# Kernel optimization log

Hardware: AMD Instinct MI355X
Metric: run time of the kernel (lower is better)

The kernel has to match this reference:

```python
import jax, jax.numpy as jnp
import numpy as np

MUL = 32          # multiplicity of 0e and 1o channels
NRAD = 8          # radial basis size
NPATH = 7         # TP instructions

# Orthonormal symmetric-traceless basis for the real l=2 irrep -> Cartesian map
_B = np.zeros((5, 3, 3))
_s2 = 1.0 / np.sqrt(2.0)
_B[0, 0, 1] = _B[0, 1, 0] = _s2                      # xy
_B[1, 1, 2] = _B[1, 2, 1] = _s2                      # yz
_B[2] = np.diag([-1.0, -1.0, 2.0]) / np.sqrt(6.0)    # 2z^2-x^2-y^2
_B[3, 0, 2] = _B[3, 2, 0] = _s2                      # xz
_B[4] = np.diag([1.0, -1.0, 0.0]) / np.sqrt(2.0)     # x^2-y^2
# w3j(1,2,1)[i,M,k], Frobenius-normalized to 1 (e3nn convention)
C121 = jnp.asarray(np.transpose(_B, (1, 0, 2)) / np.sqrt(5.0), jnp.float32)
INV_SQRT3 = float(1.0 / np.sqrt(3.0))   # w3j(1,1,0) / w3j(0,1,1) / w3j(1,0,1)
A0 = float(1.0 / np.sqrt(64.0))         # path weight, l=0 outs: sqrt(1/fan_in), fan_in=2*32
A1 = float(np.sqrt(3.0 / 96.0))         # path weight, l=1 out: sqrt((2l+1)/fan_in), fan_in=3*32


def setup_inputs() -> dict:
    key = jax.random.key(0)
    ks = jax.random.split(key, 9)
    N, E = 4096, 32768
    x = jax.random.normal(ks[0], (N, 4 * MUL), jnp.float32)
    edge_attr = jax.random.normal(ks[1], (E, 9), jnp.float32)
    edge_length = jax.random.uniform(ks[2], (E,), jnp.float32) * 5.0
    edge_src = jax.random.randint(ks[3], (E,), 0, N)
    edge_dst = jax.random.randint(ks[4], (E,), 0, N)
    W_fc1 = jax.random.normal(ks[5], (NRAD, 64), jnp.float32)
    W_fc2 = jax.random.normal(ks[6], (64, NPATH * MUL * MUL), jnp.float32)
    W_sc_s = jax.random.normal(ks[7], (MUL, MUL), jnp.float32)
    W_sc_v = jax.random.normal(ks[8], (MUL, MUL), jnp.float32)
    return dict(x=x, edge_attr=edge_attr, edge_length=edge_length,
                edge_src=edge_src, edge_dst=edge_dst,
                W_fc1=W_fc1, W_fc2=W_fc2, W_sc_s=W_sc_s, W_sc_v=W_sc_v)


def reference(x, edge_attr, edge_length, edge_src, edge_dst, W_fc1, W_fc2, W_sc_s, W_sc_v):
    N = x.shape[0]
    # radial Gaussian basis: centers linspace(0,5,8), sigma = spacing
    centers = jnp.linspace(0.0, 5.0, NRAD)
    sigma = 5.0 / (NRAD - 1)
    d = edge_length[:, None] - centers[None, :]
    radial = jnp.exp(-d * d / (2.0 * sigma * sigma))
    # radial MLP -> per-edge TP weights (e3nn FullyConnectedNet: W/sqrt(fan_in), silu)
    h = jax.nn.silu(radial @ (W_fc1 / jnp.sqrt(jnp.float32(NRAD))))
    w = h @ (W_fc2 / jnp.sqrt(jnp.float32(64)))          # [E, 7168]
    W = w.reshape(-1, NPATH, MUL, MUL)                    # [E,7,u,w]
    # split node features: 32x0e scalars + 32x1o vectors
    s = x[:, :MUL]
    v = x[:, MUL:].reshape(N, MUL, 3)
    sj = s[edge_src]                                      # [E,u]
    vj = v[edge_src]                                      # [E,u,3]
    y0 = edge_attr[:, 0]
    y1 = edge_attr[:, 1:4]
    y2 = edge_attr[:, 4:9]
    # tensor-product paths
    t00 = sj * y0[:, None]                                            # 0e x 0e
    t11 = jnp.einsum('eui,ei->eu', vj, y1) * INV_SQRT3                # 1o x 1o -> 0e
    out_s = (jnp.einsum('eu,euw->ew', t00, W[:, 0]) +
             jnp.einsum('eu,euw->ew', t11, W[:, 1])) * A0             # scalars
    out_g = (jnp.einsum('eu,euw->ew', t00, W[:, 2]) +
             jnp.einsum('eu,euw->ew', t11, W[:, 3])) * A0             # gates
    t01 = sj[:, :, None] * y1[:, None, :] * INV_SQRT3                 # 0e x 1o -> 1o
    t10 = vj * (y0[:, None, None] * INV_SQRT3)                        # 1o x 0e -> 1o
    t12 = jnp.einsum('eui,imk,em->euk', vj, C121, y2)                 # 1o x 2e -> 1o
    out_v = (jnp.einsum('euk,euw->ewk', t01, W[:, 4]) +
             jnp.einsum('euk,euw->ewk', t10, W[:, 5]) +
             jnp.einsum('euk,euw->ewk', t12, W[:, 6])) * A1           # [E,w,3]
    m_ij = jnp.concatenate([out_s, out_g, out_v.reshape(-1, 3 * MUL)], axis=1)  # [E,160]
    # scatter-mean over destination nodes
    sums = jax.ops.segment_sum(m_ij, edge_dst, num_segments=N)
    cnt = jax.ops.segment_sum(jnp.ones((m_ij.shape[0],), m_ij.dtype), edge_dst, num_segments=N)
    m_i = sums / jnp.clip(cnt, 1.0)[:, None]
    # gate: silu on scalars, sigmoid gates multiply the 1o block per-channel
    gs = jax.nn.silu(m_i[:, :MUL])
    gate = jax.nn.sigmoid(m_i[:, MUL:2 * MUL])
    gv = m_i[:, 2 * MUL:].reshape(N, MUL, 3) * gate[:, :, None]
    # residual self-connection (e3nn o3.Linear: per-irrep, / sqrt(mul_in))
    inv_sqrt_mul = 1.0 / jnp.sqrt(jnp.float32(MUL))
    h_s = gs + (s @ W_sc_s) * inv_sqrt_mul
    h_v = gv + jnp.einsum('nui,uw->nwi', v, W_sc_v) * inv_sqrt_mul
    # o3.Norm: per-irrep L2 norm over the (2l+1) components
    norm_s = jnp.sqrt(h_s * h_s + 1e-12)
    norm_v = jnp.sqrt(jnp.sum(h_v * h_v, axis=-1) + 1e-12)
    return jnp.concatenate([norm_s, norm_v], axis=1)       # [N, 64]
```

## Files before the change

kernel.cpp:

```cpp
#include <hip/hip_runtime.h>

#define NIVL  256
#define KINV  51.2f
#define KSTEP 0.01953125f
#define TPW   7168
#define BCAP  256
#define DCAP  64
#define NROW  11
#define TSTR  40
#define TPACK 448

typedef __attribute__((ext_vector_type(8))) __bf16 bf16x8;
typedef __attribute__((ext_vector_type(4))) float f32x4;
union FragU { uint4 u; bf16x8 v; };

__device__ __forceinline__ float sigmoidf_(float v) { return 1.f / (1.f + expf(-v)); }
__device__ __forceinline__ unsigned bf16r_(float x) { return (__float_as_uint(x) + 0x8000u) >> 16; }
__device__ __forceinline__ unsigned pk_(float lo, float hi) { return (bf16r_(hi) << 16) | bf16r_(lo); }

__device__ __forceinline__ f32x4 mfma_(bf16x8 a, bf16x8 b, f32x4 c) {
    return __builtin_amdgcn_mfma_f32_16x16x32_bf16(a, b, c, 0, 0, 0);
}

__global__ __launch_bounds__(256)
void prep_kernel(const float* __restrict__ W1, const float* __restrict__ W2,
                 const float* __restrict__ elen, const int* __restrict__ esrc,
                 const int* __restrict__ edst, const float* __restrict__ ea,
                 uint4* __restrict__ Bpk, int* __restrict__ cntL, int* __restrict__ cntD,
                 float* __restrict__ erec, int* __restrict__ sortedD, int E)
{
    __shared__ float hk_s[5][64];
    __shared__ float Tsl[5][1024];
    const int tid = threadIdx.x;
    const int vb = blockIdx.x;
    if (vb < TPACK) {
        const int bx = vb % 7;
        const int k0 = (vb / 7) * 4;
        for (int idx = tid; idx < 320; idx += 256) {
            int kk = idx >> 6, c = idx & 63;
            float L = (float)(k0 + kk) * KSTEP;
            float d = 0.f;
#pragma unroll
            for (int r = 0; r < 8; ++r) {
                float dd = L - (float)r * (5.f / 7.f);
                d += expf(-dd * dd * 0.98f) * W1[r * 64 + c];
            }
            d *= 0.3535533906f;
            hk_s[kk][c] = d * sigmoidf_(d) * 0.125f;
        }
        __syncthreads();
        float4 acc[5];
#pragma unroll
        for (int q = 0; q < 5; ++q) acc[q] = make_float4(0.f, 0.f, 0.f, 0.f);
        const int pw = bx * 1024 + tid * 4;
#pragma unroll 4
        for (int c = 0; c < 64; ++c) {
            float4 w4 = *(const float4*)(W2 + (size_t)c * TPW + pw);
#pragma unroll
            for (int q = 0; q < 5; ++q) {
                float hv = hk_s[q][c];
                acc[q].x = fmaf(hv, w4.x, acc[q].x);
                acc[q].y = fmaf(hv, w4.y, acc[q].y);
                acc[q].z = fmaf(hv, w4.z, acc[q].z);
                acc[q].w = fmaf(hv, w4.w, acc[q].w);
            }
        }
        __syncthreads();
#pragma unroll
        for (int q = 0; q < 5; ++q)
            *(float4*)&Tsl[q][tid * 4] = acc[q];
        __syncthreads();
        const int lane_s = tid & 63, whs = (tid >> 6) & 1, ih = tid >> 7;
        const int u0p = (lane_s >> 4) * 8, wp = whs * 16 + (lane_s & 15);
#pragma unroll
        for (int t2 = 0; t2 < 2; ++t2) {
            const int jj = k0 + ih + t2 * 2;
            const int kk = jj - k0;
            unsigned ta[4], dd[4];
#pragma unroll
            for (int q = 0; q < 4; ++q) {
                float a0 = Tsl[kk][(u0p + 2 * q) * 32 + wp];
                float a1 = Tsl[kk][(u0p + 2 * q + 1) * 32 + wp];
                float b0 = Tsl[kk + 1][(u0p + 2 * q) * 32 + wp];
                float b1 = Tsl[kk + 1][(u0p + 2 * q + 1) * 32 + wp];
                ta[q] = pk_(a0, a1);
                dd[q] = pk_(b0 - a0, b1 - a1);
            }
            Bpk[((size_t)jj * 28 + bx * 4 + whs) * 64 + lane_s]     = make_uint4(ta[0], ta[1], ta[2], ta[3]);
            Bpk[((size_t)jj * 28 + bx * 4 + 2 + whs) * 64 + lane_s] = make_uint4(dd[0], dd[1], dd[2], dd[3]);
        }
    } else {
        const float I3 = 0.5773502692f, I5 = 0.4472135955f, S2 = 0.7071067812f;
        const float I6 = 0.4082482905f, T6 = 0.8164965809f;
        int e = (vb - TPACK) * 256 + tid;
        if (e < E) {
            float t = elen[e] * KINV;
            int j = (int)t; j = j > 255 ? 255 : j;
            int pos = atomicAdd(&cntL[j], 1);
            if (pos < BCAP) {
                const float* y = ea + (size_t)e * 9;
                float y0 = y[0];
                float a = y[4], b = y[5], c = y[6], d2 = y[7], ee = y[8];
                float4 r0, r1, r2, r3;
                r0.x = t - (float)j;
                r0.y = __int_as_float(esrc[e]);
                r0.z = 0.f;
                r0.w = y0;
                r1.x = y0 * I3;
                r1.y = y[1] * I3; r1.z = y[2] * I3; r1.w = y[3] * I3;
                r2.x = (-c * I6 + ee * S2) * I5;
                r2.y = a * S2 * I5;
                r2.z = d2 * S2 * I5;
                r2.w = (-c * I6 - ee * S2) * I5;
                r3.x = b * S2 * I5;
                r3.y = c * T6 * I5;
                r3.z = 0.f; r3.w = 0.f;
                float4* dst = (float4*)(erec + ((size_t)j * BCAP + pos) * 16);
                dst[0] = r0; dst[1] = r1; dst[2] = r2; dst[3] = r3;
            }
            int slot = j * BCAP + (pos < BCAP ? pos : BCAP - 1);
            int d = edst[e];
            int pd = atomicAdd(&cntD[d], 1);
            if (pd < DCAP) sortedD[d * DCAP + pd] = slot;
        }
    }
}

__global__ __launch_bounds__(128, 2)
void fold_kernel(const float* __restrict__ x, const int* __restrict__ cntL,
                 const float* __restrict__ erec, const uint4* __restrict__ Bpk,
                 float* __restrict__ msg)
{
    const int j = blockIdx.x >> 2, qtr = blockIdx.x & 3;
    __shared__ __align__(16) unsigned short TB[NROW * 16 * TSTR];
    __shared__ float ECF[16];
    const int tid = threadIdx.x;

    const int cnt = min(cntL[j], BCAP);
    const int nchunk = (cnt + 15) >> 4;
    const int te = tid & 15, sub = tid >> 4;
    const int wh = tid >> 6, lane = tid & 63;
    const int col = lane & 15, quad = lane >> 4;

    float4 er0 = {0,0,0,0}, er1 = {0,0,0,0}, er2 = {0,0,0,0}, er3 = {0,0,0,0};
    if (qtr < nchunk) {
        int ce = min(16, cnt - (qtr << 4));
        if (te < ce) {
            const float4* rp = (const float4*)(erec + ((size_t)j * BCAP + (qtr << 4) + te) * 16);
            er0 = rp[0]; er1 = rp[1]; er2 = rp[2]; er3 = rp[3];
        }
    }

    bf16x8 Bt[7][2];
    {
        const uint4* bp = Bpk + (size_t)j * 28 * 64 + lane;
#pragma unroll
        for (int pl = 0; pl < 7; ++pl) {
            FragU fa; fa.u = bp[(pl * 4 + wh) * 64];     Bt[pl][0] = fa.v;
            FragU fd; fd.u = bp[(pl * 4 + 2 + wh) * 64]; Bt[pl][1] = fd.v;
        }
    }

    const float A0 = 0.125f, A1 = 0.1767766953f;

    for (int ci = qtr; ci < nchunk; ci += 4) {
        const int base = ci << 4;
        const int cntE = min(16, cnt - base);

        const int u0 = sub * 4;
        float s4[4], vvx[12];
        if (te < cntE) {
            int src = __float_as_int(er0.y);
            const float* xp = x + (size_t)src * 128;
            *(float4*)s4 = *(const float4*)(xp + u0);
            *(float4*)(vvx)     = *(const float4*)(xp + 32 + 3 * u0);
            *(float4*)(vvx + 4) = *(const float4*)(xp + 32 + 3 * u0 + 4);
            *(float4*)(vvx + 8) = *(const float4*)(xp + 32 + 3 * u0 + 8);
        }
        float4 nr0 = {0,0,0,0}, nr1 = {0,0,0,0}, nr2 = {0,0,0,0}, nr3 = {0,0,0,0};
        const int cin = ci + 4;
        if (cin < nchunk) {
            int ce2 = min(16, cnt - (cin << 4));
            if (te < ce2) {
                const float4* rp = (const float4*)(erec + ((size_t)j * BCAP + (cin << 4) + te) * 16);
                nr0 = rp[0]; nr1 = rp[1]; nr2 = rp[2]; nr3 = rp[3];
            }
        }

        __syncthreads();

        {
            float rv[NROW][4];
            if (te < cntE) {
                float y0 = er0.w;
                float y0i = er1.x, y1i0 = er1.y, y1i1 = er1.z, y1i2 = er1.w;
                float M0 = er2.x, M1 = er2.y, M2 = er2.z, M4 = er2.w;
                float M5 = er3.x, M8 = er3.y;
                if (sub == 0) ECF[te] = er0.x;
#pragma unroll
                for (int up = 0; up < 4; ++up) {
                    float s = s4[up];
                    float v0 = vvx[3 * up], v1 = vvx[3 * up + 1], v2 = vvx[3 * up + 2];
                    rv[0][up] = s * y0;
                    rv[1][up] = v0 * y1i0 + v1 * y1i1 + v2 * y1i2;
                    rv[2][up] = s * y1i0;
                    rv[3][up] = s * y1i1;
                    rv[4][up] = s * y1i2;
                    rv[5][up] = v0 * y0i;
                    rv[6][up] = v1 * y0i;
                    rv[7][up] = v2 * y0i;
                    rv[8][up]  = v0 * M0 + v1 * M1 + v2 * M2;
                    rv[9][up]  = v0 * M1 + v1 * M4 + v2 * M5;
                    rv[10][up] = v0 * M2 + v1 * M5 + v2 * M8;
                }
            } else {
#pragma unroll
                for (int r = 0; r < NROW; ++r)
#pragma unroll
                    for (int up = 0; up < 4; ++up) rv[r][up] = 0.f;
            }
#pragma unroll
            for (int r = 0; r < NROW; ++r) {
                unsigned lo = pk_(rv[r][0], rv[r][1]);
                unsigned hi = pk_(rv[r][2], rv[r][3]);
                *(uint2*)&TB[(r * 16 + te) * TSTR + u0] = make_uint2(lo, hi);
            }
        }
        __syncthreads();

        f32x4 cS0 = {0,0,0,0}, cS1 = {0,0,0,0}, cG0 = {0,0,0,0}, cG1 = {0,0,0,0};
        f32x4 cV[3][2];
#pragma unroll
        for (int k = 0; k < 3; ++k) { cV[k][0] = (f32x4){0,0,0,0}; cV[k][1] = (f32x4){0,0,0,0}; }

        #define LOADA(r) ({ FragU fa_; fa_.u = *(const uint4*)&TB[((r) * 16 + col) * TSTR + quad * 8]; fa_.v; })

        bf16x8 a0 = LOADA(0), a1 = LOADA(1);
        cS0 = mfma_(a0, Bt[0][0], cS0); cS0 = mfma_(a1, Bt[1][0], cS0);
        cS1 = mfma_(a0, Bt[0][1], cS1); cS1 = mfma_(a1, Bt[1][1], cS1);
        cG0 = mfma_(a0, Bt[2][0], cG0); cG0 = mfma_(a1, Bt[3][0], cG0);
        cG1 = mfma_(a0, Bt[2][1], cG1); cG1 = mfma_(a1, Bt[3][1], cG1);
#pragma unroll
        for (int k = 0; k < 3; ++k) {
            bf16x8 ak;
            ak = LOADA(2 + k);
            cV[k][0] = mfma_(ak, Bt[4][0], cV[k][0]);
            cV[k][1] = mfma_(ak, Bt[4][1], cV[k][1]);
            ak = LOADA(5 + k);
            cV[k][0] = mfma_(ak, Bt[5][0], cV[k][0]);
            cV[k][1] = mfma_(ak, Bt[5][1], cV[k][1]);
            ak = LOADA(8 + k);
            cV[k][0] = mfma_(ak, Bt[6][0], cV[k][0]);
            cV[k][1] = mfma_(ak, Bt[6][1], cV[k][1]);
        }

        const int w = wh * 16 + col;
        const int sbase = j * BCAP + base;
#pragma unroll
        for (int reg = 0; reg < 4; ++reg) {
            int e = quad * 4 + reg;
            if (e < cntE) {
                float f = ECF[e];
                float* mp = msg + (size_t)(sbase + e) * 160;
                mp[w]            = (cS0[reg] + f * cS1[reg]) * A0;
                mp[32 + w]       = (cG0[reg] + f * cG1[reg]) * A0;
                mp[64 + 3 * w]     = (cV[0][0][reg] + f * cV[0][1][reg]) * A1;
                mp[64 + 3 * w + 1] = (cV[1][0][reg] + f * cV[1][1][reg]) * A1;
                mp[64 + 3 * w + 2] = (cV[2][0][reg] + f * cV[2][1][reg]) * A1;
            }
        }
        #undef LOADA
        er0 = nr0; er1 = nr1; er2 = nr2; er3 = nr3;
    }
}

__global__ __launch_bounds__(256)
void node_kernel(const float* __restrict__ x, const float* __restrict__ Wss,
                 const float* __restrict__ Wsv, const float* __restrict__ msg,
                 const int* __restrict__ sortedD, const int* __restrict__ cntD,
                 float* __restrict__ out, int N)
{
    __shared__ float ms[8][160];
    const int tid = threadIdx.x;
    const int n0 = blockIdx.x * 8;
    const float IM = 0.1767766953f;

#pragma unroll
    for (int it = 0; it < 5; ++it) {
        int task = tid + it * 256;
        int nl = task / 160;
        int c = task - nl * 160;
        int n = n0 + nl;
        if (n < N) {
            int cd = cntD[n];
            int cc = cd < DCAP ? cd : DCAP;
            const int* sp = sortedD + n * DCAP;
            float s = 0.f;
            for (int i0 = 0; i0 < cc; i0 += 8) {
                int4 ia = *(const int4*)(sp + i0);
                int4 ib = *(const int4*)(sp + i0 + 4);
                int id[8] = { ia.x, ia.y, ia.z, ia.w, ib.x, ib.y, ib.z, ib.w };
                float p[8];
#pragma unroll
                for (int k = 0; k < 8; ++k)
                    p[k] = (i0 + k < cc) ? msg[(size_t)id[k] * 160 + c] : 0.f;
#pragma unroll
                for (int k = 0; k < 8; ++k) s += p[k];
            }
            ms[nl][c] = s / fmaxf((float)cd, 1.f);
        }
    }
    __syncthreads();

#pragma unroll
    for (int it = 0; it < 2; ++it) {
        int task = tid + it * 256;
        int nl = task >> 6, col = task & 63;
        int n = n0 + nl;
        if (n >= N) continue;
        const float* m  = ms[nl];
        const float* xp = x + (size_t)n * 128;
        if (col < 32) {
            int w = col;
            float mval = m[w];
            float gs = mval * sigmoidf_(mval);
            float dot = 0.f;
#pragma unroll 4
            for (int u = 0; u < 32; ++u) dot += xp[u] * Wss[u * 32 + w];
            float hs = gs + dot * IM;
            out[(size_t)n * 64 + w] = sqrtf(hs * hs + 1e-12f);
        } else {
            int w = col - 32;
            float gate = sigmoidf_(m[32 + w]);
            float g0 = m[64 + 3 * w + 0] * gate;
            float g1 = m[64 + 3 * w + 1] * gate;
            float g2 = m[64 + 3 * w + 2] * gate;
            float d0 = 0.f, d1 = 0.f, d2 = 0.f;
#pragma unroll 4
            for (int u = 0; u < 32; ++u) {
                float wvv = Wsv[u * 32 + w];
                d0 += xp[32 + 3 * u + 0] * wvv;
                d1 += xp[32 + 3 * u + 1] * wvv;
                d2 += xp[32 + 3 * u + 2] * wvv;
            }
            float h0 = g0 + d0 * IM, h1 = g1 + d1 * IM, h2 = g2 + d2 * IM;
            out[(size_t)n * 64 + 32 + w] = sqrtf(h0 * h0 + h1 * h1 + h2 * h2 + 1e-12f);
        }
    }
}

extern "C" void kernel_launch(void* const* d_in, const int* in_sizes, int n_in,
                              void* d_out, int out_size, void* d_ws, size_t ws_size,
                              hipStream_t stream)
{
    const float* x    = (const float*)d_in[0];
    const float* ea   = (const float*)d_in[1];
    const float* elen = (const float*)d_in[2];
    const int*   esrc = (const int*)d_in[3];
    const int*   edst = (const int*)d_in[4];
    const float* W1   = (const float*)d_in[5];
    const float* W2   = (const float*)d_in[6];
    const float* Wss  = (const float*)d_in[7];
    const float* Wsv  = (const float*)d_in[8];
    float* out = (float*)d_out;

    const int N = in_sizes[0] / 128;
    const int E = in_sizes[2];

    float* Bpkf   = (float*)d_ws;
    float* msg    = Bpkf + (size_t)256 * 28 * 64 * 4;
    float* erec   = msg + (size_t)256 * BCAP * 160;
    int*   cntL   = (int*)(erec + (size_t)256 * BCAP * 16);
    int*   cntD   = cntL + 256;
    int*   sortedD= cntD + N;
    uint4* Bpk    = (uint4*)Bpkf;

    hipMemsetAsync(cntL, 0, (size_t)(256 + N) * sizeof(int), stream);

    prep_kernel<<<TPACK + (E + 255) / 256, 256, 0, stream>>>(W1, W2, elen, esrc, edst, ea, Bpk, cntL, cntD, erec, sortedD, E);
    fold_kernel<<<NIVL * 4, 128, 0, stream>>>(x, cntL, erec, Bpk, msg);
    node_kernel<<<(N + 7) / 8, 256, 0, stream>>>(x, Wss, Wsv, msg, sortedD, cntD, out, N);
}
```

Before: 135.7 us.

## Build MFMA A-fragments in registers with single-wave fold blocks, removing LDS staging

The fold kernel now uses one 64-lane wave per block, and each lane builds its 8-wide bf16 A-fragment for all 11 rows directly in registers. The shared-memory transpose buffer, the two __syncthreads per chunk and the LDS edge-factor array are gone; the edge factor is broadcast with a wave shuffle instead. Each wave computes both 16-column output halves, so it holds twice the B fragments in registers. The grid grows to 8 blocks per interval, and the software prefetch of the next chunk's edge records is dropped. Register pressure per lane rises.

Measured after the change: 139.6 us. 2.9% more time.

```diff
diff --git a/kernel.cpp b/kernel.cpp
--- a/kernel.cpp
+++ b/kernel.cpp
@@ -7,7 +7,6 @@
 #define BCAP  256
 #define DCAP  64
 #define NROW  11
-#define TSTR  40
 #define TPACK 448
 
 typedef __attribute__((ext_vector_type(8))) __bf16 bf16x8;
@@ -126,81 +125,69 @@
     }
 }
 
-__global__ __launch_bounds__(128, 2)
+__global__ __launch_bounds__(64, 2)
 void fold_kernel(const float* __restrict__ x, const int* __restrict__ cntL,
                  const float* __restrict__ erec, const uint4* __restrict__ Bpk,
                  float* __restrict__ msg)
 {
-    const int j = blockIdx.x >> 2, qtr = blockIdx.x & 3;
-    __shared__ __align__(16) unsigned short TB[NROW * 16 * TSTR];
-    __shared__ float ECF[16];
-    const int tid = threadIdx.x;
+    const int j = blockIdx.x >> 3, off = blockIdx.x & 7;
+    const int lane = threadIdx.x;
+    const int em = lane & 15;
+    const int quad = lane >> 4;
+    const int u0 = quad * 8;
 
     const int cnt = min(cntL[j], BCAP);
     const int nchunk = (cnt + 15) >> 4;
-    const int te = tid & 15, sub = tid >> 4;
-    const int wh = tid >> 6, lane = tid & 63;
-    const int col = lane & 15, quad = lane >> 4;
-
-    float4 er0 = {0,0,0,0}, er1 = {0,0,0,0}, er2 = {0,0,0,0}, er3 = {0,0,0,0};
-    if (qtr < nchunk) {
-        int ce = min(16, cnt - (qtr << 4));
-        if (te < ce) {
-            const float4* rp = (const float4*)(erec + ((size_t)j * BCAP + (qtr << 4) + te) * 16);
-            er0 = rp[0]; er1 = rp[1]; er2 = rp[2]; er3 = rp[3];
-        }
-    }
-
-    bf16x8 Bt[7][2];
+    if (off >= nchunk) return;
+
+    bf16x8 Bt[7][2][2];
     {
         const uint4* bp = Bpk + (size_t)j * 28 * 64 + lane;
 #pragma unroll
         for (int pl = 0; pl < 7; ++pl) {
-            FragU fa; fa.u = bp[(pl * 4 + wh) * 64];     Bt[pl][0] = fa.v;
-            FragU fd; fd.u = bp[(pl * 4 + 2 + wh) * 64]; Bt[pl][1] = fd.v;
+#pragma unroll
+            for (int wh = 0; wh < 2; ++wh) {
+                FragU fa; fa.u = bp[(pl * 4 + wh) * 64];     Bt[pl][0][wh] = fa.v;
+                FragU fd; fd.u = bp[(pl * 4 + 2 + wh) * 64]; Bt[pl][1][wh] = fd.v;
+            }
         }
     }
 
     const float A0 = 0.125f, A1 = 0.1767766953f;
 
-    for (int ci = qtr; ci < nchunk; ci += 4) {
+    for (int ci = off; ci < nchunk; ci += 8) {
         const int base = ci << 4;
         const int cntE = min(16, cnt - base);
 
-        const int u0 = sub * 4;
-        float s4[4], vvx[12];
-        if (te < cntE) {
+        float4 er0 = {0,0,0,0}, er1 = {0,0,0,0}, er2 = {0,0,0,0}, er3 = {0,0,0,0};
+        if (em < cntE) {
+            const float4* rp = (const float4*)(erec + ((size_t)j * BCAP + base + em) * 16);
+            er0 = rp[0]; er1 = rp[1]; er2 = rp[2]; er3 = rp[3];
+        }
+
+        float s8[8], vv[24];
+        if (em < cntE) {
             int src = __float_as_int(er0.y);
             const float* xp = x + (size_t)src * 128;
-            *(float4*)s4 = *(const float4*)(xp + u0);
-            *(float4*)(vvx)     = *(const float4*)(xp + 32 + 3 * u0);
-            *(float4*)(vvx + 4) = *(const float4*)(xp + 32 + 3 * u0 + 4);
-            *(float4*)(vvx + 8) = *(const float4*)(xp + 32 + 3 * u0 + 8);
-        }
-        float4 nr0 = {0,0,0,0}, nr1 = {0,0,0,0}, nr2 = {0,0,0,0}, nr3 = {0,0,0,0};
-        const int cin = ci + 4;
-        if (cin < nchunk) {
-            int ce2 = min(16, cnt - (cin << 4));
-            if (te < ce2) {
-                const float4* rp = (const float4*)(erec + ((size_t)j * BCAP + (cin << 4) + te) * 16);
-                nr0 = rp[0]; nr1 = rp[1]; nr2 = rp[2]; nr3 = rp[3];
-            }
-        }
-
-        __syncthreads();
-
+            *(float4*)(s8)     = *(const float4*)(xp + u0);
+            *(float4*)(s8 + 4) = *(const float4*)(xp + u0 + 4);
+#pragma unroll
+            for (int q = 0; q < 6; ++q)
+                *(float4*)(vv + 4 * q) = *(const float4*)(xp + 32 + 3 * u0 + 4 * q);
+        }
+
+        bf16x8 pa[NROW];
         {
-            float rv[NROW][4];
-            if (te < cntE) {
-                float y0 = er0.w;
-                float y0i = er1.x, y1i0 = er1.y, y1i1 = er1.z, y1i2 = er1.w;
-                float M0 = er2.x, M1 = er2.y, M2 = er2.z, M4 = er2.w;
-                float M5 = er3.x, M8 = er3.y;
-                if (sub == 0) ECF[te] = er0.x;
-#pragma unroll
-                for (int up = 0; up < 4; ++up) {
-                    float s = s4[up];
-                    float v0 = vvx[3 * up], v1 = vvx[3 * up + 1], v2 = vvx[3 * up + 2];
+            float y0 = er0.w;
+            float y0i = er1.x, y1i0 = er1.y, y1i1 = er1.z, y1i2 = er1.w;
+            float M0 = er2.x, M1 = er2.y, M2 = er2.z, M4 = er2.w;
+            float M5 = er3.x, M8 = er3.y;
+            float rv[NROW][8];
+            if (em < cntE) {
+#pragma unroll
+                for (int up = 0; up < 8; ++up) {
+                    float s = s8[up];
+                    float v0 = vv[3 * up], v1 = vv[3 * up + 1], v2 = vv[3 * up + 2];
                     rv[0][up] = s * y0;
                     rv[1][up] = v0 * y1i0 + v1 * y1i1 + v2 * y1i2;
                     rv[2][up] = s * y1i0;
@@ -217,60 +204,56 @@
 #pragma unroll
                 for (int r = 0; r < NROW; ++r)
 #pragma unroll
-                    for (int up = 0; up < 4; ++up) rv[r][up] = 0.f;
+                    for (int up = 0; up < 8; ++up) rv[r][up] = 0.f;
             }
 #pragma unroll
             for (int r = 0; r < NROW; ++r) {
-                unsigned lo = pk_(rv[r][0], rv[r][1]);
-                unsigned hi = pk_(rv[r][2], rv[r][3]);
-                *(uint2*)&TB[(r * 16 + te) * TSTR + u0] = make_uint2(lo, hi);
-            }
-        }
-        __syncthreads();
-
-        f32x4 cS0 = {0,0,0,0}, cS1 = {0,0,0,0}, cG0 = {0,0,0,0}, cG1 = {0,0,0,0};
-        f32x4 cV[3][2];
-#pragma unroll
-        for (int k = 0; k < 3; ++k) { cV[k][0] = (f32x4){0,0,0,0}; cV[k][1] = (f32x4){0,0,0,0}; }
-
-        #define LOADA(r) ({ FragU fa_; fa_.u = *(const uint4*)&TB[((r) * 16 + col) * TSTR + quad * 8]; fa_.v; })
-
-        bf16x8 a0 = LOADA(0), a1 = LOADA(1);
-        cS0 = mfma_(a0, Bt[0][0], cS0); cS0 = mfma_(a1, Bt[1][0], cS0);
-        cS1 = mfma_(a0, Bt[0][1], cS1); cS1 = mfma_(a1, Bt[1][1], cS1);
-        cG0 = mfma_(a0, Bt[2][0], cG0); cG0 = mfma_(a1, Bt[3][0], cG0);
-        cG1 = mfma_(a0, Bt[2][1], cG1); cG1 = mfma_(a1, Bt[3][1], cG1);
-#pragma unroll
-        for (int k = 0; k < 3; ++k) {
-            bf16x8 ak;
-            ak = LOADA(2 + k);
-            cV[k][0] = mfma_(ak, Bt[4][0], cV[k][0]);
-            cV[k][1] = mfma_(ak, Bt[4][1], cV[k][1]);
-            ak = LOADA(5 + k);
-            cV[k][0] = mfma_(ak, Bt[5][0], cV[k][0]);
-            cV[k][1] = mfma_(ak, Bt[5][1], cV[k][1]);
-            ak = LOADA(8 + k);
-            cV[k][0] = mfma_(ak, Bt[6][0], cV[k][0]);
-            cV[k][1] = mfma_(ak, Bt[6][1], cV[k][1]);
-        }
-
-        const int w = wh * 16 + col;
+                FragU f;
+                f.u = make_uint4(pk_(rv[r][0], rv[r][1]), pk_(rv[r][2], rv[r][3]),
+                                 pk_(rv[r][4], rv[r][5]), pk_(rv[r][6], rv[r][7]));
+                pa[r] = f.v;
+            }
+        }
+
+        const float fr = er0.x;
         const int sbase = j * BCAP + base;
-#pragma unroll
-        for (int reg = 0; reg < 4; ++reg) {
-            int e = quad * 4 + reg;
-            if (e < cntE) {
-                float f = ECF[e];
-                float* mp = msg + (size_t)(sbase + e) * 160;
-                mp[w]            = (cS0[reg] + f * cS1[reg]) * A0;
-                mp[32 + w]       = (cG0[reg] + f * cG1[reg]) * A0;
-                mp[64 + 3 * w]     = (cV[0][0][reg] + f * cV[0][1][reg]) * A1;
-                mp[64 + 3 * w + 1] = (cV[1][0][reg] + f * cV[1][1][reg]) * A1;
-                mp[64 + 3 * w + 2] = (cV[2][0][reg] + f * cV[2][1][reg]) * A1;
-            }
-        }
-        #undef LOADA
-        er0 = nr0; er1 = nr1; er2 = nr2; er3 = nr3;
+
+#pragma unroll
+        for (int wh = 0; wh < 2; ++wh) {
+            f32x4 cS0 = {0,0,0,0}, cS1 = {0,0,0,0}, cG0 = {0,0,0,0}, cG1 = {0,0,0,0};
+            f32x4 cV[3][2];
+#pragma unroll
+            for (int k = 0; k < 3; ++k) { cV[k][0] = (f32x4){0,0,0,0}; cV[k][1] = (f32x4){0,0,0,0}; }
+
+            cS0 = mfma_(pa[0], Bt[0][0][wh], cS0); cS0 = mfma_(pa[1], Bt[1][0][wh], cS0);
+            cS1 = mfma_(pa[0], Bt[0][1][wh], cS1); cS1 = mfma_(pa[1], Bt[1][1][wh], cS1);
+            cG0 = mfma_(pa[0], Bt[2][0][wh], cG0); cG0 = mfma_(pa[1], Bt[3][0][wh], cG0);
+            cG1 = mfma_(pa[0], Bt[2][1][wh], cG1); cG1 = mfma_(pa[1], Bt[3][1][wh], cG1);
+#pragma unroll
+            for (int k = 0; k < 3; ++k) {
+                cV[k][0] = mfma_(pa[2 + k], Bt[4][0][wh], cV[k][0]);
+                cV[k][1] = mfma_(pa[2 + k], Bt[4][1][wh], cV[k][1]);
+                cV[k][0] = mfma_(pa[5 + k], Bt[5][0][wh], cV[k][0]);
+                cV[k][1] = mfma_(pa[5 + k], Bt[5][1][wh], cV[k][1]);
+                cV[k][0] = mfma_(pa[8 + k], Bt[6][0][wh], cV[k][0]);
+                cV[k][1] = mfma_(pa[8 + k], Bt[6][1][wh], cV[k][1]);
+            }
+
+            const int w = wh * 16 + em;
+#pragma unroll
+            for (int reg = 0; reg < 4; ++reg) {
+                int e = quad * 4 + reg;
+                float f = __shfl(fr, e);
+                if (e < cntE) {
+                    float* mp = msg + (size_t)(sbase + e) * 160;
+                    mp[w]            = (cS0[reg] + f * cS1[reg]) * A0;
+                    mp[32 + w]       = (cG0[reg] + f * cG1[reg]) * A0;
+                    mp[64 + 3 * w]     = (cV[0][0][reg] + f * cV[0][1][reg]) * A1;
+                    mp[64 + 3 * w + 1] = (cV[1][0][reg] + f * cV[1][1][reg]) * A1;
+                    mp[64 + 3 * w + 2] = (cV[2][0][reg] + f * cV[2][1][reg]) * A1;
+                }
+            }
+        }
     }
 }
 
@@ -378,6 +361,6 @@
     hipMemsetAsync(cntL, 0, (size_t)(256 + N) * sizeof(int), stream);
 
     prep_kernel<<<TPACK + (E + 255) / 256, 256, 0, stream>>>(W1, W2, elen, esrc, edst, ea, Bpk, cntL, cntD, erec, sortedD, E);
-    fold_kernel<<<NIVL * 4, 128, 0, stream>>>(x, cntL, erec, Bpk, msg);
+    fold_kernel<<<NIVL * 8, 64, 0, stream>>>(x, cntL, erec, Bpk, msg);
     node_kernel<<<(N + 7) / 8, 256, 0, stream>>>(x, Wss, Wsv, msg, sortedD, cntD, out, N);
 }
```
